# Performance work log

Measured on AMD Instinct MI355X. Metric: run time of the kernel, lower is better.

## Reference

```python
import jax, jax.numpy as jnp
import numpy as np

B, N = 256, 2000          # clouds, points per cloud
M1, M2 = 100, 5           # fps sample counts (ratio 0.05 twice)
K1, K2 = 20, 20           # neighbors per cluster (= 1/ratio)
R1, R2, R3 = 0.3, 1.0, 2.0
F1, F2, F3 = 5, 25, 45


def _fps(pts, m):
    # iterative farthest point sampling, deterministic start at index 0
    n = pts.shape[0]
    def step(carry, _):
        mind, last = carry
        d = jnp.sum((pts - pts[last]) ** 2, axis=-1)
        mind = jnp.minimum(mind, d)
        return (mind, jnp.argmax(mind).astype(jnp.int32)), last
    _, idx = jax.lax.scan(step, (jnp.full((n,), 1e10, pts.dtype), jnp.int32(0)), None, length=m)
    return idx


def _radius_knn(q, pts, k, r):
    # k nearest neighbors of each query, masked to the radius ball (static-shape gnn.radius)
    d = jnp.sum((q[:, None, :] - pts[None, :, :]) ** 2, axis=-1)  # (M, n)
    negd, idx = jax.lax.top_k(-d, k)
    return idx, (-negd) <= r * r


def _masked_max(h, mask):
    return jnp.max(jnp.where(mask[..., None], h, -1e10), axis=1)


def _forward(points, W1, b1, W2, b2, W3, b3, D1, bD1, D2, bD2, D3, bD3):
    def per_cloud(pts):
        # ---- encode level 1 ----
        samples = pts[_fps(pts, M1)]                              # (M1,3)
        idx1, m1 = _radius_knn(samples, pts, K1, R1)
        rel = (pts[idx1] - samples[:, None, :]) / R1 * m1[..., None]   # (M1,K1,3)
        f1 = _masked_max(jax.nn.relu(rel @ W1 + b1), m1)          # (M1,F1)
        # ---- encode level 2 ----
        samples2 = samples[_fps(samples, M2)]                     # (M2,3)
        idx2, m2 = _radius_knn(samples2, samples, K2, R2)
        rel2 = (samples[idx2] - samples2[:, None, :]) / R2 * m2[..., None]
        h2 = jax.nn.relu(jnp.concatenate([rel2, f1[idx2]], axis=-1) @ W2 + b2)
        f2 = _masked_max(h2, m2)                                  # (M2,F2)
        # ---- encode level 3 (global) ----
        rel3 = samples2 / R3
        h3 = jax.nn.relu(jnp.concatenate([rel3, f2], axis=-1) @ W3 + b3)
        latent = jnp.max(h3, axis=0)                              # (F3,)
        # ---- hierarchical decode ----
        o1 = (latent @ D1 + bD1).reshape(M2, 3 + F2)
        dec, cf = o1[:, :3], jax.nn.relu(o1[:, 3:])               # (M2,3),(M2,F2)
        o2 = (cf @ D2 + bD2).reshape(M2 * K2, 3 + F1)
        dec2, cf2 = o2[:, :3], jax.nn.relu(o2[:, 3:])             # (M2*K2,3/F1)
        dec3 = (cf2 @ D3 + bD3).reshape(M2 * K2 * K1, 3)
        # ---- reconstruction: repeat_interleave + add + scale ----
        s2_out = dec * R3
        s_out = (jnp.repeat(s2_out, K2, axis=0) + dec2) * R2
        return (jnp.repeat(s_out, K1, axis=0) + dec3) * R1        # (N,3)
    return jax.vmap(per_cloud)(points).reshape(B * N, 3)


def setup_inputs():
    key = jax.random.key(0)
    ks = jax.random.split(key, 8)
    p = lambda k, s: jax.random.normal(k, s, jnp.float32) * 0.1
    z = lambda s: jnp.zeros((s,), jnp.float32)
    return {
        "points": jax.random.normal(ks[0], (B, N, 3), jnp.float32),
        "W1": p(ks[1], (3, F1)), "b1": z(F1),
        "W2": p(ks[2], (3 + F1, F2)), "b2": z(F2),
        "W3": p(ks[3], (3 + F2, F3)), "b3": z(F3),
        "D1": p(ks[4], (F3, M2 * (3 + F2))), "bD1": z(M2 * (3 + F2)),
        "D2": p(ks[5], (F2, K2 * (3 + F1))), "bD2": z(K2 * (3 + F1)),
        "D3": p(ks[6], (F1, K1 * 3)), "bD3": z(K1 * 3),
    }


def reference(points, W1, b1, W2, b2, W3, b3, D1, bD1, D2, bD2, D3, bD3):
    return _forward(points, W1, b1, W2, b2, W3, b3, D1, bD1, D2, bD2, D3, bD3)
```

## Files before the change

### kernel.cpp

```cpp
#include <hip/hip_runtime.h>

#define TPB 512
#define NW 8
#define NPTS 2000
#define M1C 100
#define M2C 5
#define KNN 20
#define CANDCAP 128

__device__ __forceinline__ float dist3(float px, float py, float pz,
                                       float qx, float qy, float qz) {
#pragma clang fp contract(off)
    float dx = px - qx, dy = py - qy, dz = pz - qz;
    return dx * dx + dy * dy + dz * dz;
}

#define ARGMAX_STEP(ctrl, rm)                                                        \
    do {                                                                             \
        float ov = __int_as_float(__builtin_amdgcn_update_dpp(                       \
            (int)0xff800000, __float_as_int(v), ctrl, rm, 0xf, false));              \
        int oi = __builtin_amdgcn_update_dpp(0x7fffffff, i, ctrl, rm, 0xf, false);   \
        bool take = (ov > v) || (ov == v && oi < i);                                 \
        v = take ? ov : v;                                                           \
        i = take ? oi : i;                                                           \
    } while (0)

__device__ __forceinline__ void wave_argmax(float& v, int& i) {
    ARGMAX_STEP(0x111, 0xf);
    ARGMAX_STEP(0x112, 0xf);
    ARGMAX_STEP(0x114, 0xf);
    ARGMAX_STEP(0x118, 0xf);
    ARGMAX_STEP(0x142, 0xa);
    ARGMAX_STEP(0x143, 0xc);
    v = __int_as_float(__builtin_amdgcn_readlane(__float_as_int(v), 63));
    i = __builtin_amdgcn_readlane(i, 63);
}

#define FMAX_STEP(ctrl, rm)                                                          \
    do {                                                                             \
        float _t = __int_as_float(__builtin_amdgcn_update_dpp(                       \
            (int)0xff800000, __float_as_int(x), ctrl, rm, 0xf, false));              \
        x = fmaxf(x, _t);                                                            \
    } while (0)

__device__ __forceinline__ float wave_fmax(float x) {
    FMAX_STEP(0x111, 0xf);
    FMAX_STEP(0x112, 0xf);
    FMAX_STEP(0x114, 0xf);
    FMAX_STEP(0x118, 0xf);
    FMAX_STEP(0x142, 0xa);
    FMAX_STEP(0x143, 0xc);
    return __int_as_float(__builtin_amdgcn_readlane(__float_as_int(x), 63));
}

__global__ __launch_bounds__(TPB, 2) void fused_kernel(
    const float* __restrict__ P,
    const float* __restrict__ W1, const float* __restrict__ b1,
    const float* __restrict__ W2, const float* __restrict__ b2,
    const float* __restrict__ W3, const float* __restrict__ b3,
    const float* __restrict__ D1, const float* __restrict__ bD1,
    const float* __restrict__ D2, const float* __restrict__ bD2,
    const float* __restrict__ D3, const float* __restrict__ bD3,
    float* __restrict__ out)
{
    __shared__ float sP[3][NPTS];
    __shared__ float smpx[M1C], smpy[M1C], smpz[M1C];
    __shared__ float s2x[M2C], s2y[M2C], s2z[M2C];
    __shared__ float f1s[M1C][5];
    __shared__ float knd[NW][CANDCAP];
    __shared__ int   kni[NW][CANDCAP];
    __shared__ __align__(16) float4 sA[2][4];
    __shared__ __align__(16) float  sZ[2][4];
    __shared__ int flags[4];
    __shared__ float f2s[M2C][25];
    __shared__ float latent[45];
    __shared__ float decv[M2C][3];
    __shared__ float cfs[M2C][25];
    __shared__ float dec2s[M1C][3];
    __shared__ float cf2s[M1C][5];
    __shared__ float w2s[200], b2s[25], w3s[1260], b3s[45];

    const int b = blockIdx.x;
    const int tid = threadIdx.x;
    const int lane = tid & 63;
    const int wid = tid >> 6;
    float* sx = sP[0]; float* sy = sP[1]; float* sz = sP[2];

    const float R1SQ = (float)(0.3 * 0.3);
    const float R2SQ = 1.0f;
    const float INVR1 = 1.0f / 0.3f;

    const float* Pb = P + (size_t)b * (NPTS * 3);
    const float4* P4 = (const float4*)Pb;
    for (int i = tid; i < (NPTS * 3) / 4; i += TPB) {
        float4 f = P4[i];
        int j = 4 * i;
        float v[4] = {f.x, f.y, f.z, f.w};
#pragma unroll
        for (int e = 0; e < 4; ++e) {
            int jj = j + e;
            (&sP[0][0])[(jj % 3) * NPTS + jj / 3] = v[e];
        }
    }
    for (int t = tid; t < 200; t += TPB) w2s[t] = W2[t];
    for (int t = tid; t < 25; t += TPB) b2s[t] = b2[t];
    for (int t = tid; t < 1260; t += TPB) w3s[t] = W3[t];
    for (int t = tid; t < 45; t += TPB) b3s[t] = b3[t];
    if (tid < 4) flags[tid] = 0;
    __syncthreads();

    if (wid < 4) {
        float px[8], py[8], pz[8], mind[8];
#pragma unroll
        for (int k = 0; k < 8; ++k) {
            int j = tid + (k << 8);
            bool v = j < NPTS;
            int jc = v ? j : 0;
            px[k] = v ? sx[jc] : 1e18f;
            py[k] = v ? sy[jc] : 1e18f;
            pz[k] = v ? sz[jc] : 1e18f;
            mind[k] = v ? 1e10f : -1.0f;
        }

        float qx = sx[0], qy = sy[0], qz = sz[0];
        for (int it = 0; it < M1C; ++it) {
            if (tid == 0) { smpx[it] = qx; smpy[it] = qy; smpz[it] = qz; }
            float bv = -1.0f; int bi = 0x7fffffff;
#pragma unroll
            for (int k = 0; k < 8; ++k) {
                float d = dist3(px[k], py[k], pz[k], qx, qy, qz);
                float m = fminf(mind[k], d);
                mind[k] = m;
                if (m > bv) { bv = m; bi = tid + (k << 8); }
            }
            if (it == M1C - 1) {
                if (lane == 0)
                    __hip_atomic_store(&flags[wid], M1C, __ATOMIC_RELEASE,
                                       __HIP_MEMORY_SCOPE_WORKGROUP);
                break;
            }
            float lv = bv; int li = bi;
            wave_argmax(bv, bi);
            int p = it & 1;
            if (lv == bv && li == bi) {
                int k = bi >> 8;
                float cx = px[0], cy = py[0], cz = pz[0];
#pragma unroll
                for (int kk = 1; kk < 8; ++kk) {
                    bool t = (k == kk);
                    cx = t ? px[kk] : cx;
                    cy = t ? py[kk] : cy;
                    cz = t ? pz[kk] : cz;
                }
                sA[p][wid] = make_float4(bv, __int_as_float(bi), cx, cy);
                sZ[p][wid] = cz;
            }
            if (lane == 0)
                __hip_atomic_store(&flags[wid], it + 1, __ATOMIC_RELEASE,
                                   __HIP_MEMORY_SCOPE_WORKGROUP);
            for (;;) {
                int f = 0x7fffffff;
                if (lane < 4)
                    f = __hip_atomic_load(&flags[lane], __ATOMIC_ACQUIRE,
                                          __HIP_MEMORY_SCOPE_WORKGROUP);
                if (__ballot(f >= it + 1) == ~0ull) break;
                __builtin_amdgcn_s_sleep(1);
            }
            float4 a0 = sA[p][0], a1 = sA[p][1], a2 = sA[p][2], a3 = sA[p][3];
            float4 z0 = *(const float4*)&sZ[p][0];
            float cv = a0.x; int ci = __float_as_int(a0.y);
            qx = a0.z; qy = a0.w; qz = z0.x;
#define SEL(aw, zz)                                                                  \
            {                                                                        \
                int ii = __float_as_int(aw.y);                                       \
                bool t = (aw.x > cv) || (aw.x == cv && ii < ci);                     \
                if (t) { cv = aw.x; ci = ii; qx = aw.z; qy = aw.w; qz = zz; }        \
            }
            SEL(a1, z0.y) SEL(a2, z0.z) SEL(a3, z0.w)
#undef SEL
        }

        if (wid == 0) {
            float ax = smpx[lane], ay = smpy[lane], az = smpz[lane];
            bool vb2 = lane < (M1C - 64);
            float bx2 = vb2 ? smpx[lane + 64] : 1e18f;
            float by2 = vb2 ? smpy[lane + 64] : 1e18f;
            float bz2 = vb2 ? smpz[lane + 64] : 1e18f;
            float m2a = 1e10f;
            float m2b = vb2 ? 1e10f : -1.0f;
            int last2 = 0;
            for (int it = 0; it < M2C; ++it) {
                float fx = smpx[last2], fy = smpy[last2], fz = smpz[last2];
                if (lane == 0) { s2x[it] = fx; s2y[it] = fy; s2z[it] = fz; }
                m2a = fminf(m2a, dist3(ax, ay, az, fx, fy, fz));
                m2b = fminf(m2b, dist3(bx2, by2, bz2, fx, fy, fz));
                float v = m2a; int i = lane;
                if (m2b > v) { v = m2b; i = lane + 64; }
                wave_argmax(v, i);
                last2 = i;
            }
        }
    } else {
        float rw1[15], rb1[5];
#pragma unroll
        for (int i = 0; i < 15; ++i) rw1[i] = W1[i];
#pragma unroll
        for (int i = 0; i < 5; ++i) rb1[i] = b1[i];

        for (int s = wid - 4; s < M1C; s += 4) {
            while (__hip_atomic_load(&flags[0], __ATOMIC_ACQUIRE,
                                     __HIP_MEMORY_SCOPE_WORKGROUP) <= s)
                __builtin_amdgcn_s_sleep(2);
            float qx = smpx[s], qy = smpy[s], qz = smpz[s];
            int cn = 0;
#pragma unroll 4
            for (int c = 0; c < 32; ++c) {
                int j = c * 64 + lane;
                float d = 0.0f; bool pred = false;
                if (j < NPTS) {
                    d = dist3(sx[j], sy[j], sz[j], qx, qy, qz);
                    pred = (d <= R1SQ);
                }
                unsigned long long mb = __ballot(pred);
                if (pred) {
                    int pos = cn + (int)__popcll(mb & ((1ull << lane) - 1ull));
                    if (pos < CANDCAP) { knd[wid][pos] = d; kni[wid][pos] = j; }
                }
                cn += (int)__popcll(mb);
            }
            if (cn > CANDCAP) cn = CANDCAP;
            float fmx[5];
#pragma unroll
            for (int f = 0; f < 5; ++f) fmx[f] = -1e30f;
            for (int t = lane; t < cn; t += 64) {
                float d = knd[wid][t]; int j = kni[wid][t];
                bool valid = true;
                if (cn > KNN) {
                    int rank = 0;
                    for (int u = 0; u < cn; ++u) {
                        float du = knd[wid][u]; int iu = kni[wid][u];
                        rank += (du < d || (du == d && iu < j)) ? 1 : 0;
                    }
                    valid = rank < KNN;
                }
                if (valid) {
                    float rx = (sx[j] - qx) * INVR1;
                    float ry = (sy[j] - qy) * INVR1;
                    float rz = (sz[j] - qz) * INVR1;
#pragma unroll
                    for (int f = 0; f < 5; ++f) {
                        float h = fmaf(rx, rw1[f], fmaf(ry, rw1[5 + f], fmaf(rz, rw1[10 + f], rb1[f])));
                        fmx[f] = fmaxf(fmx[f], fmaxf(h, 0.0f));
                    }
                }
            }
#pragma unroll
            for (int f = 0; f < 5; ++f) fmx[f] = wave_fmax(fmx[f]);
            if (lane == 0) {
#pragma unroll
                for (int f = 0; f < 5; ++f) f1s[s][f] = fmx[f];
            }
        }
    }
    __syncthreads();

    for (int s = wid; s < M2C; s += NW) {
        float qx2 = s2x[s], qy2 = s2y[s], qz2 = s2z[s];
        int cn = 0;
#pragma unroll
        for (int c = 0; c < 2; ++c) {
            int j = c * 64 + lane;
            float d = 0.0f; bool pred = false;
            if (j < M1C) {
                d = dist3(smpx[j], smpy[j], smpz[j], qx2, qy2, qz2);
                pred = (d <= R2SQ);
            }
            unsigned long long mb = __ballot(pred);
            if (pred) {
                int pos = cn + (int)__popcll(mb & ((1ull << lane) - 1ull));
                knd[wid][pos] = d; kni[wid][pos] = j;
            }
            cn += (int)__popcll(mb);
        }
        float hmx[25];
#pragma unroll
        for (int f = 0; f < 25; ++f) hmx[f] = -1e30f;
        for (int t = lane; t < cn; t += 64) {
            float d = knd[wid][t]; int j = kni[wid][t];
            bool valid = true;
            if (cn > KNN) {
                int rank = 0;
                for (int u = 0; u < cn; ++u) {
                    float du = knd[wid][u]; int iu = kni[wid][u];
                    rank += (du < d || (du == d && iu < j)) ? 1 : 0;
                }
                valid = rank < KNN;
            }
            if (valid) {
                float in8[8];
                in8[0] = smpx[j] - qx2; in8[1] = smpy[j] - qy2; in8[2] = smpz[j] - qz2;
#pragma unroll
                for (int f = 0; f < 5; ++f) in8[3 + f] = f1s[j][f];
#pragma unroll
                for (int f = 0; f < 25; ++f) {
                    float h = b2s[f];
#pragma unroll
                    for (int i = 0; i < 8; ++i) h = fmaf(in8[i], w2s[i * 25 + f], h);
                    hmx[f] = fmaxf(hmx[f], fmaxf(h, 0.0f));
                }
            }
        }
#pragma unroll
        for (int f = 0; f < 25; ++f) {
            float mx = wave_fmax(hmx[f]);
            if (lane == 0) f2s[s][f] = mx;
        }
    }
    __syncthreads();

    if (wid == 0 && lane < 45) {
        float lm = -1e30f;
        for (int r = 0; r < M2C; ++r) {
            float h = b3s[lane];
            h = fmaf(s2x[r] * 0.5f, w3s[0 * 45 + lane], h);
            h = fmaf(s2y[r] * 0.5f, w3s[1 * 45 + lane], h);
            h = fmaf(s2z[r] * 0.5f, w3s[2 * 45 + lane], h);
#pragma unroll
            for (int i = 0; i < 25; ++i) h = fmaf(f2s[r][i], w3s[(3 + i) * 45 + lane], h);
            lm = fmaxf(lm, fmaxf(h, 0.0f));
        }
        latent[lane] = lm;
    }
    __syncthreads();

    for (int t = tid; t < 140; t += TPB) {
        float acc = bD1[t];
        for (int i = 0; i < 45; i++) acc = fmaf(latent[i], D1[i * 140 + t], acc);
        int r = t / 28, c = t % 28;
        if (c < 3) decv[r][c] = acc;
        else cfs[r][c - 3] = fmaxf(acc, 0.0f);
    }
    __syncthreads();

    for (int t = tid; t < 800; t += TPB) {
        int r = t / 160, c = t % 160;
        float acc = bD2[c];
        for (int i = 0; i < 25; i++) acc = fmaf(cfs[r][i], D2[i * 160 + c], acc);
        int g = r * 20 + c / 8, c8 = c % 8;
        if (c8 < 3) dec2s[g][c8] = acc;
        else cf2s[g][c8 - 3] = fmaxf(acc, 0.0f);
    }
    __syncthreads();

    float* outb = out + (size_t)b * (NPTS * 3);
    for (int t = tid; t < NPTS * 3; t += TPB) {
        int n = t / 3, c = t % 3;
        int g = n / 20;
        int m = n / 400;
        int r60 = (n % 20) * 3 + c;
        float acc = bD3[r60];
        for (int i = 0; i < 5; i++) acc = fmaf(cf2s[g][i], D3[i * 60 + r60], acc);
        float val = ((decv[m][c] * 2.0f + dec2s[g][c]) + acc) * 0.3f;
        outb[t] = val;
    }
}

extern "C" void kernel_launch(void* const* d_in, const int* in_sizes, int n_in,
                              void* d_out, int out_size, void* d_ws, size_t ws_size,
                              hipStream_t stream) {
    const float* P   = (const float*)d_in[0];
    const float* W1  = (const float*)d_in[1];
    const float* b1  = (const float*)d_in[2];
    const float* W2  = (const float*)d_in[3];
    const float* b2  = (const float*)d_in[4];
    const float* W3  = (const float*)d_in[5];
    const float* b3  = (const float*)d_in[6];
    const float* D1  = (const float*)d_in[7];
    const float* bD1 = (const float*)d_in[8];
    const float* D2  = (const float*)d_in[9];
    const float* bD2 = (const float*)d_in[10];
    const float* D3  = (const float*)d_in[11];
    const float* bD3 = (const float*)d_in[12];
    float* out = (float*)d_out;

    int B = in_sizes[0] / (NPTS * 3);
    hipLaunchKernelGGL(fused_kernel, dim3(B), dim3(TPB), 0, stream,
                       P, W1, b1, W2, b2, W3, b3, D1, bD1, D2, bD2, D3, bD3, out);
}
```

Before: 205.2 us.

## Prioritize FPS waves, pack points as float4, and shorten argmax dependency chains

Stores cloud points in shared memory as float4 (AoS) so each point is read with one 128-bit LDS load instead of three scalar loads. Raises scheduling priority of the four FPS waves with s_setprio and removes the sleep in their spin-wait, so the serial farthest-point loop is less delayed by the kNN consumer waves. It also replaces the sequential per-thread and cross-wave argmax selections with tree-shaped reductions to shorten dependency chains. The float4 layout uses a third more LDS, and busy spinning without sleep may take issue slots from the other waves.

```diff
diff --git a/kernel.cpp b/kernel.cpp
--- a/kernel.cpp
+++ b/kernel.cpp
@@ -63,7 +63,7 @@
     const float* __restrict__ D3, const float* __restrict__ bD3,
     float* __restrict__ out)
 {
-    __shared__ float sP[3][NPTS];
+    __shared__ __align__(16) float4 sP4[NPTS];
     __shared__ float smpx[M1C], smpy[M1C], smpz[M1C];
     __shared__ float s2x[M2C], s2y[M2C], s2z[M2C];
     __shared__ float f1s[M1C][5];
@@ -84,7 +84,6 @@
     const int tid = threadIdx.x;
     const int lane = tid & 63;
     const int wid = tid >> 6;
-    float* sx = sP[0]; float* sy = sP[1]; float* sz = sP[2];
 
     const float R1SQ = (float)(0.3 * 0.3);
     const float R2SQ = 1.0f;
@@ -94,12 +93,13 @@
     const float4* P4 = (const float4*)Pb;
     for (int i = tid; i < (NPTS * 3) / 4; i += TPB) {
         float4 f = P4[i];
-        int j = 4 * i;
+        int base = 4 * i;
         float v[4] = {f.x, f.y, f.z, f.w};
 #pragma unroll
         for (int e = 0; e < 4; ++e) {
-            int jj = j + e;
-            (&sP[0][0])[(jj % 3) * NPTS + jj / 3] = v[e];
+            int fi = base + e;
+            int pt = fi / 3, c = fi - 3 * pt;
+            ((float*)&sP4[pt])[c] = v[e];
         }
     }
     for (int t = tid; t < 200; t += TPB) w2s[t] = W2[t];
@@ -110,29 +110,35 @@
     __syncthreads();
 
     if (wid < 4) {
+        __builtin_amdgcn_s_setprio(3);
         float px[8], py[8], pz[8], mind[8];
 #pragma unroll
         for (int k = 0; k < 8; ++k) {
             int j = tid + (k << 8);
             bool v = j < NPTS;
-            int jc = v ? j : 0;
-            px[k] = v ? sx[jc] : 1e18f;
-            py[k] = v ? sy[jc] : 1e18f;
-            pz[k] = v ? sz[jc] : 1e18f;
+            float4 p = v ? sP4[j] : make_float4(1e18f, 1e18f, 1e18f, 0.0f);
+            px[k] = p.x; py[k] = p.y; pz[k] = p.z;
             mind[k] = v ? 1e10f : -1.0f;
         }
 
-        float qx = sx[0], qy = sy[0], qz = sz[0];
+        float qx = sP4[0].x, qy = sP4[0].y, qz = sP4[0].z;
         for (int it = 0; it < M1C; ++it) {
             if (tid == 0) { smpx[it] = qx; smpy[it] = qy; smpz[it] = qz; }
-            float bv = -1.0f; int bi = 0x7fffffff;
+            float m[8];
 #pragma unroll
             for (int k = 0; k < 8; ++k) {
                 float d = dist3(px[k], py[k], pz[k], qx, qy, qz);
-                float m = fminf(mind[k], d);
-                mind[k] = m;
-                if (m > bv) { bv = m; bi = tid + (k << 8); }
-            }
+                m[k] = fminf(mind[k], d);
+                mind[k] = m[k];
+            }
+            float va = m[0]; int ka = 0; if (m[1] > va) { va = m[1]; ka = 1; }
+            float vb = m[2]; int kb = 2; if (m[3] > vb) { vb = m[3]; kb = 3; }
+            float vc = m[4]; int kc = 4; if (m[5] > vc) { vc = m[5]; kc = 5; }
+            float vd = m[6]; int kd = 6; if (m[7] > vd) { vd = m[7]; kd = 7; }
+            if (vb > va) { va = vb; ka = kb; }
+            if (vd > vc) { vc = vd; kc = kd; }
+            if (vc > va) { va = vc; ka = kc; }
+            float bv = va; int bi = tid + (ka << 8);
             if (it == M1C - 1) {
                 if (lane == 0)
                     __hip_atomic_store(&flags[wid], M1C, __ATOMIC_RELEASE,
@@ -164,20 +170,25 @@
                     f = __hip_atomic_load(&flags[lane], __ATOMIC_ACQUIRE,
                                           __HIP_MEMORY_SCOPE_WORKGROUP);
                 if (__ballot(f >= it + 1) == ~0ull) break;
-                __builtin_amdgcn_s_sleep(1);
             }
             float4 a0 = sA[p][0], a1 = sA[p][1], a2 = sA[p][2], a3 = sA[p][3];
             float4 z0 = *(const float4*)&sZ[p][0];
-            float cv = a0.x; int ci = __float_as_int(a0.y);
-            qx = a0.z; qy = a0.w; qz = z0.x;
-#define SEL(aw, zz)                                                                  \
-            {                                                                        \
-                int ii = __float_as_int(aw.y);                                       \
-                bool t = (aw.x > cv) || (aw.x == cv && ii < ci);                     \
-                if (t) { cv = aw.x; ci = ii; qx = aw.z; qy = aw.w; qz = zz; }        \
-            }
-            SEL(a1, z0.y) SEL(a2, z0.z) SEL(a3, z0.w)
-#undef SEL
+            float cv0 = a0.x; int ci0 = __float_as_int(a0.y);
+            float x0 = a0.z, y0 = a0.w, zz0 = z0.x;
+            {
+                int ii = __float_as_int(a1.y);
+                bool t = (a1.x > cv0) || (a1.x == cv0 && ii < ci0);
+                if (t) { cv0 = a1.x; ci0 = ii; x0 = a1.z; y0 = a1.w; zz0 = z0.y; }
+            }
+            float cv1 = a2.x; int ci1 = __float_as_int(a2.y);
+            float x1 = a2.z, y1 = a2.w, zz1 = z0.z;
+            {
+                int ii = __float_as_int(a3.y);
+                bool t = (a3.x > cv1) || (a3.x == cv1 && ii < ci1);
+                if (t) { cv1 = a3.x; ci1 = ii; x1 = a3.z; y1 = a3.w; zz1 = z0.w; }
+            }
+            bool t = (cv1 > cv0) || (cv1 == cv0 && ci1 < ci0);
+            qx = t ? x1 : x0; qy = t ? y1 : y0; qz = t ? zz1 : zz0;
         }
 
         if (wid == 0) {
@@ -200,7 +211,9 @@
                 last2 = i;
             }
         }
+        __builtin_amdgcn_s_setprio(0);
     } else {
+        __builtin_amdgcn_s_setprio(0);
         float rw1[15], rb1[5];
 #pragma unroll
         for (int i = 0; i < 15; ++i) rw1[i] = W1[i];
@@ -218,7 +231,8 @@
                 int j = c * 64 + lane;
                 float d = 0.0f; bool pred = false;
                 if (j < NPTS) {
-                    d = dist3(sx[j], sy[j], sz[j], qx, qy, qz);
+                    float4 p = sP4[j];
+                    d = dist3(p.x, p.y, p.z, qx, qy, qz);
                     pred = (d <= R1SQ);
                 }
                 unsigned long long mb = __ballot(pred);
@@ -244,9 +258,10 @@
                     valid = rank < KNN;
                 }
                 if (valid) {
-                    float rx = (sx[j] - qx) * INVR1;
-                    float ry = (sy[j] - qy) * INVR1;
-                    float rz = (sz[j] - qz) * INVR1;
+                    float4 p = sP4[j];
+                    float rx = (p.x - qx) * INVR1;
+                    float ry = (p.y - qy) * INVR1;
+                    float rz = (p.z - qz) * INVR1;
 #pragma unroll
                     for (int f = 0; f < 5; ++f) {
                         float h = fmaf(rx, rw1[f], fmaf(ry, rw1[5 + f], fmaf(rz, rw1[10 + f], rb1[f])));
```

Measured after the change: 202.4 us. No clear change (-1.3%).
